# Kernel optimization log

Measured on AMD Instinct MI355X. Metric: run time of the kernel, lower is better.

## Reference

```python
import jax, jax.numpy as jnp
import numpy as np

NEG_SLOPE = 0.2
LN_EPS = 1e-5


def setup_inputs() -> dict:
    key = jax.random.key(0)
    k1, k2, k3, k4 = jax.random.split(key, 4)
    N, E, Din, Dout = 50000, 1000000, 64, 64
    h = jax.random.normal(k1, (N, Din), dtype=jnp.float32)
    edge_index = jax.random.randint(k2, (2, E), 0, N, dtype=jnp.int32)
    # Linear(in_dim, out_dim, bias=False): weight [Dout, Din]
    W = jax.random.normal(k3, (Dout, Din), dtype=jnp.float32) / np.sqrt(Din)
    # attention vector a: [1, 2*Dout] (xavier-normal-ish scale)
    a = jax.random.normal(k4, (1, 2 * Dout), dtype=jnp.float32) * 0.1
    ln_gamma = jnp.ones((Dout,), dtype=jnp.float32)
    ln_beta = jnp.zeros((Dout,), dtype=jnp.float32)
    return {"h": h, "edge_index": edge_index, "W": W, "a": a,
            "ln_gamma": ln_gamma, "ln_beta": ln_beta}


def reference(h, edge_index, W, a, ln_gamma, ln_beta):
    N, Dout = h.shape[0], W.shape[0]
    src, dst = edge_index[0], edge_index[1]
    hW = h @ W.T  # [N, Dout]
    # score_e = leakyrelu([h_src || h_dst] . a) = leakyrelu(s1[src] + s2[dst])
    a1, a2 = a[0, :Dout], a[0, Dout:]
    s1 = hW @ a1  # [N]
    s2 = hW @ a2  # [N]
    e = jax.nn.leaky_relu(s1[src] + s2[dst], NEG_SLOPE)  # [E]
    # softmax grouped by source node (segment softmax), numerically stable
    m = jax.ops.segment_max(e, src, num_segments=N)  # [N]
    ex = jnp.exp(e - m[src])
    denom = jax.ops.segment_sum(ex, src, num_segments=N)  # [N]
    att = ex / denom[src]  # [E]  (dropout: eval mode, identity)
    # scatter-add weighted source features into destination nodes
    msg = att[:, None] * hW[src]  # [E, Dout]
    h_prime = jnp.zeros_like(hW).at[dst].add(msg)
    # residual + LayerNorm
    x = hW + h_prime
    mu = jnp.mean(x, axis=-1, keepdims=True)
    var = jnp.var(x, axis=-1, keepdims=True)
    return (x - mu) * jax.lax.rsqrt(var + LN_EPS) * ln_gamma + ln_beta
```

## Files before the change

### kernel.cpp

```cpp
#include <hip/hip_runtime.h>
#include <hip/hip_bf16.h>

#define NEG_SLOPE 0.2f
#define LN_EPS 1e-5f
#define D 64
#define BSH 6
#define BNODES 64
#define NBMAX 1024
#define BCAP 1792
#define SSH 8
#define NSBMAX 256
#define SCAP 6144
#define OVFCAP 65536

typedef unsigned long long u64;
typedef unsigned int u32;
typedef unsigned short u16;

__device__ __forceinline__ u16 f2bf(float f) {
    u32 u = __float_as_uint(f);
    return (u16)((u + 0x7FFFu + ((u >> 16) & 1u)) >> 16);
}
__device__ __forceinline__ float bf_lo(u32 p) { return __uint_as_float(p << 16); }
__device__ __forceinline__ float bf_hi(u32 p) { return __uint_as_float(p & 0xFFFF0000u); }

__global__ void __launch_bounds__(256, 4)
k_hw_scores(const float* __restrict__ h,
            const float* __restrict__ W,
            const float* __restrict__ a,
            float* __restrict__ hW,
            u16* __restrict__ hWb,
            float* __restrict__ s1,
            float* __restrict__ s2,
            int N) {
    const int lane = threadIdx.x & 63;
    const int wid  = threadIdx.x >> 6;
    const int wavesPerBlock = blockDim.x >> 6;
    const int nWaves = gridDim.x * wavesPerBlock;

    float wcol[D];
    {
        const float4* wr = (const float4*)(W + (size_t)lane * D);
        #pragma unroll
        for (int q = 0; q < D / 4; ++q) {
            float4 w4 = wr[q];
            wcol[q * 4 + 0] = w4.x; wcol[q * 4 + 1] = w4.y;
            wcol[q * 4 + 2] = w4.z; wcol[q * 4 + 3] = w4.w;
        }
    }
    const float a1l = a[lane];
    const float a2l = a[D + lane];

    for (int i = blockIdx.x * wavesPerBlock + wid; i < N; i += nWaves) {
        const int iu = __builtin_amdgcn_readfirstlane(i);
        const float* hr = h + (size_t)iu * D;

        float acc0 = 0.f, acc1 = 0.f, acc2 = 0.f, acc3 = 0.f;
        #pragma unroll
        for (int k = 0; k < D; k += 4) {
            acc0 = fmaf(hr[k + 0], wcol[k + 0], acc0);
            acc1 = fmaf(hr[k + 1], wcol[k + 1], acc1);
            acc2 = fmaf(hr[k + 2], wcol[k + 2], acc2);
            acc3 = fmaf(hr[k + 3], wcol[k + 3], acc3);
        }
        float c = (acc0 + acc1) + (acc2 + acc3);
        hW[(size_t)iu * D + lane] = c;
        hWb[(size_t)iu * D + lane] = f2bf(c);

        float p1 = c * a1l;
        float p2 = c * a2l;
        #pragma unroll
        for (int off = 32; off > 0; off >>= 1) {
            p1 += __shfl_xor(p1, off, 64);
            p2 += __shfl_xor(p2, off, 64);
        }
        if (lane == 0) { s1[iu] = p1; s2[iu] = p2; }
    }
}

__device__ __forceinline__ float edge_ex(float v1, float v2) {
    float x = v1 + v2;
    float e = x > 0.f ? x : NEG_SLOPE * x;
    return expf(fminf(e, 60.f));
}

__global__ void __launch_bounds__(1024)
k_bin(const int* __restrict__ src,
      const int* __restrict__ dst,
      const float* __restrict__ s1,
      const float* __restrict__ s2,
      float* __restrict__ denom,
      int* __restrict__ dcnt_g,
      u32* __restrict__ drecs,
      int* __restrict__ scnt_g,
      u32* __restrict__ srecs,
      u32* __restrict__ ovf_rec,
      int* __restrict__ ovf_dst,
      int* __restrict__ ovf_n,
      int E, int nb, int nsb) {
    const int TPB = 1024, EPT = 4;
    __shared__ int lcnt[NBMAX], lbase[NBMAX], lfill[NBMAX];
    __shared__ int scnt[NSBMAX], sbase[NSBMAX], sfill[NSBMAX];

    const int chunk = blockIdx.x * (TPB * EPT);
    for (int i = threadIdx.x; i < nb; i += TPB)  { lcnt[i] = 0; lfill[i] = 0; }
    for (int i = threadIdx.x; i < nsb; i += TPB) { scnt[i] = 0; sfill[i] = 0; }
    __syncthreads();

    int sv[EPT], dv[EPT];
    const int e0 = chunk + threadIdx.x * EPT;
    if (e0 + EPT <= E) {
        int4 s4 = *(const int4*)(src + e0);
        int4 d4 = *(const int4*)(dst + e0);
        sv[0] = s4.x; sv[1] = s4.y; sv[2] = s4.z; sv[3] = s4.w;
        dv[0] = d4.x; dv[1] = d4.y; dv[2] = d4.z; dv[3] = d4.w;
    } else {
        #pragma unroll
        for (int j = 0; j < EPT; ++j) {
            int i = e0 + j;
            sv[j] = (i < E) ? src[i] : 0;
            dv[j] = (i < E) ? dst[i] : -1;
        }
    }

    #pragma unroll
    for (int j = 0; j < EPT; ++j) {
        if (dv[j] >= 0) {
            atomicAdd(&lcnt[dv[j] >> BSH], 1);
            atomicAdd(&scnt[sv[j] >> SSH], 1);
        }
    }
    __syncthreads();

    for (int b = threadIdx.x; b < nb; b += TPB) {
        int l = lcnt[b];
        if (l) lbase[b] = atomicAdd(&dcnt_g[b], l);
    }
    for (int b = threadIdx.x; b < nsb; b += TPB) {
        int l = scnt[b];
        if (l) sbase[b] = atomicAdd(&scnt_g[b], l);
    }
    __syncthreads();

    #pragma unroll
    for (int j = 0; j < EPT; ++j) {
        int d_ = dv[j];
        if (d_ < 0) continue;
        int s = sv[j];

        int b = d_ >> BSH;
        u32 drec = (u32)s | ((u32)(d_ & (BNODES - 1)) << 16);
        int r = lbase[b] + atomicAdd(&lfill[b], 1);
        if (r < BCAP) {
            drecs[(size_t)b * BCAP + r] = drec;
        } else {
            int o = atomicAdd(ovf_n, 1);
            if (o < OVFCAP) { ovf_rec[o] = drec; ovf_dst[o] = d_; }
        }

        int sb = s >> SSH;
        u32 srec = (u32)s | ((u32)d_ << 16);
        int rs = sbase[sb] + atomicAdd(&sfill[sb], 1);
        if (rs < SCAP) {
            srecs[(size_t)sb * SCAP + rs] = srec;
        } else {
            atomicAdd(&denom[s], edge_ex(s1[s], s2[d_]));
        }
    }
}

__global__ void __launch_bounds__(512)
k_denom(const u32* __restrict__ srecs,
        const int* __restrict__ scnt_g,
        const float* __restrict__ s1,
        const float* __restrict__ s2,
        float* __restrict__ denom,
        int N) {
    __shared__ float acc[256];
    const int b = blockIdx.x;
    const int tid = threadIdx.x;
    if (tid < 256) acc[tid] = 0.f;
    __syncthreads();

    const int total = min(scnt_g[b], SCAP);
    const u32* base = srecs + (size_t)b * SCAP;
    for (int i = tid; i < total; i += 512) {
        u32 r = base[i];
        int s = r & 0xFFFF;
        int d = r >> 16;
        atomicAdd(&acc[s & 255], edge_ex(s1[s], s2[d]));
    }
    __syncthreads();

    if (tid < 256) {
        int g = (b << SSH) + tid;
        if (g < N) denom[g] += acc[tid];
    }
}

__global__ void __launch_bounds__(512)
k_bucket_agg(const u32* __restrict__ drecs,
             const int* __restrict__ dcnt_g,
             const float* __restrict__ s1,
             const float* __restrict__ s2,
             const float* __restrict__ denom,
             const float* __restrict__ hW,
             const u16* __restrict__ hWb,
             const float* __restrict__ gamma,
             const float* __restrict__ beta,
             const u32* __restrict__ ovf_rec,
             const int* __restrict__ ovf_dst,
             const int* __restrict__ ovf_n_p,
             float* __restrict__ out,
             int N) {
    __shared__ u64 ro[BCAP];
    __shared__ float s2l[BNODES];
    __shared__ int hh[BNODES], oo[BNODES], cc[BNODES];

    const int b    = blockIdx.x;
    const int tid  = threadIdx.x;
    const int lane = tid & 63;
    const int wid  = tid >> 6;
    const int g    = lane >> 4;
    const int li   = lane & 15;
    const int node0 = b << BSH;
    const int nn    = min(BNODES, N - node0);
    const int total = min(dcnt_g[b], BCAP);

    if (tid < nn) s2l[tid] = s2[node0 + tid];
    if (tid < BNODES) hh[tid] = 0;
    __syncthreads();

    u64 rr[4]; bool valid[4];
    const u32* base = drecs + (size_t)b * BCAP;
    #pragma unroll
    for (int q = 0; q < 4; ++q) {
        int idx = tid + q * 512;
        valid[q] = idx < total;
        u32 r = valid[q] ? base[idx] : 0u;
        if (valid[q]) {
            int s  = r & 0xFFFF;
            int dl = (r >> 16) & (BNODES - 1);
            float att = edge_ex(s1[s], s2l[dl]) / denom[s];
            rr[q] = ((u64)__float_as_uint(att) << 32) | (u64)r;
            atomicAdd(&hh[dl], 1);
        } else rr[q] = 0;
    }
    __syncthreads();

    if (tid < BNODES) oo[tid] = hh[tid];
    __syncthreads();
    for (int off = 1; off < BNODES; off <<= 1) {
        int t = 0;
        if (tid < BNODES && tid >= off) t = oo[tid - off];
        __syncthreads();
        if (tid < BNODES) oo[tid] += t;
        __syncthreads();
    }
    if (tid < BNODES) { int e_ = oo[tid] - hh[tid]; oo[tid] = e_; cc[tid] = e_; }
    __syncthreads();

    #pragma unroll
    for (int q = 0; q < 4; ++q) if (valid[q])
        ro[atomicAdd(&cc[((u32)rr[q] >> 16) & (BNODES - 1)], 1)] = rr[q];
    __syncthreads();

    int ovn = *ovf_n_p;
    if (ovn > OVFCAP) ovn = OVFCAP;

    #pragma unroll
    for (int k = 0; k < 8; ++k) {
        int nl = (wid << 3) + k;
        if (nl >= nn) break;
        int beg = oo[nl], end = cc[nl];

        float ax = 0.f, ay = 0.f, az = 0.f, aw = 0.f;
        for (int p = beg; p < end; p += 16) {
            float at0 = 0.f, at1 = 0.f, at2 = 0.f, at3 = 0.f;
            int s0 = 0, s1i = 0, s2i = 0, s3 = 0;
            int i0 = p + g, i1 = p + 4 + g, i2 = p + 8 + g, i3 = p + 12 + g;
            if (i0 < end) { u64 r2 = ro[i0]; s0  = (u32)r2 & 0xFFFF; at0 = __uint_as_float((u32)(r2 >> 32)); }
            if (i1 < end) { u64 r2 = ro[i1]; s1i = (u32)r2 & 0xFFFF; at1 = __uint_as_float((u32)(r2 >> 32)); }
            if (i2 < end) { u64 r2 = ro[i2]; s2i = (u32)r2 & 0xFFFF; at2 = __uint_as_float((u32)(r2 >> 32)); }
            if (i3 < end) { u64 r2 = ro[i3]; s3  = (u32)r2 & 0xFFFF; at3 = __uint_as_float((u32)(r2 >> 32)); }
            const uint2 v0 = *(const uint2*)(hWb + (size_t)s0  * D + li * 4);
            const uint2 v1 = *(const uint2*)(hWb + (size_t)s1i * D + li * 4);
            const uint2 v2 = *(const uint2*)(hWb + (size_t)s2i * D + li * 4);
            const uint2 v3 = *(const uint2*)(hWb + (size_t)s3  * D + li * 4);
            ax = fmaf(at0, bf_lo(v0.x), ax); ay = fmaf(at0, bf_hi(v0.x), ay);
            az = fmaf(at0, bf_lo(v0.y), az); aw = fmaf(at0, bf_hi(v0.y), aw);
            ax = fmaf(at1, bf_lo(v1.x), ax); ay = fmaf(at1, bf_hi(v1.x), ay);
            az = fmaf(at1, bf_lo(v1.y), az); aw = fmaf(at1, bf_hi(v1.y), aw);
            ax = fmaf(at2, bf_lo(v2.x), ax); ay = fmaf(at2, bf_hi(v2.x), ay);
            az = fmaf(at2, bf_lo(v2.y), az); aw = fmaf(at2, bf_hi(v2.y), aw);
            ax = fmaf(at3, bf_lo(v3.x), ax); ay = fmaf(at3, bf_hi(v3.x), ay);
            az = fmaf(at3, bf_lo(v3.y), az); aw = fmaf(at3, bf_hi(v3.y), aw);
        }

        for (int r = 0; r < ovn; ++r) {
            if (ovf_dst[r] != node0 + nl) continue;
            if (g == 0) {
                u32 r2 = ovf_rec[r];
                int s = r2 & 0xFFFF;
                float att = edge_ex(s1[s], s2l[nl]) / denom[s];
                const uint2 v = *(const uint2*)(hWb + (size_t)s * D + li * 4);
                ax = fmaf(att, bf_lo(v.x), ax); ay = fmaf(att, bf_hi(v.x), ay);
                az = fmaf(att, bf_lo(v.y), az); aw = fmaf(att, bf_hi(v.y), aw);
            }
        }

        ax += __shfl_xor(ax, 16, 64); ax += __shfl_xor(ax, 32, 64);
        ay += __shfl_xor(ay, 16, 64); ay += __shfl_xor(ay, 32, 64);
        az += __shfl_xor(az, 16, 64); az += __shfl_xor(az, 32, 64);
        aw += __shfl_xor(aw, 16, 64); aw += __shfl_xor(aw, 32, 64);

        const float4 hv = *(const float4*)(hW + (size_t)(node0 + nl) * D + li * 4);
        float x0 = hv.x + ax, x1 = hv.y + ay, x2 = hv.z + az, x3 = hv.w + aw;

        float sm = x0 + x1 + x2 + x3;
        sm += __shfl_xor(sm, 1, 64); sm += __shfl_xor(sm, 2, 64);
        sm += __shfl_xor(sm, 4, 64); sm += __shfl_xor(sm, 8, 64);
        float mu = sm * (1.f / D);
        float d0 = x0 - mu, d1 = x1 - mu, d2 = x2 - mu, d3 = x3 - mu;
        float vv = d0 * d0 + d1 * d1 + d2 * d2 + d3 * d3;
        vv += __shfl_xor(vv, 1, 64); vv += __shfl_xor(vv, 2, 64);
        vv += __shfl_xor(vv, 4, 64); vv += __shfl_xor(vv, 8, 64);
        float inv = rsqrtf(vv * (1.f / D) + LN_EPS);

        if (g == 0) {
            const float4 gm = *(const float4*)(gamma + li * 4);
            const float4 bt = *(const float4*)(beta + li * 4);
            float4 o;
            o.x = d0 * inv * gm.x + bt.x;
            o.y = d1 * inv * gm.y + bt.y;
            o.z = d2 * inv * gm.z + bt.z;
            o.w = d3 * inv * gm.w + bt.w;
            *(float4*)(out + (size_t)(node0 + nl) * D + li * 4) = o;
        }
    }
}

static inline size_t align256(size_t x) { return (x + 255) & ~size_t(255); }

extern "C" void kernel_launch(void* const* d_in, const int* in_sizes, int n_in,
                              void* d_out, int out_size, void* d_ws, size_t ws_size,
                              hipStream_t stream) {
    const float* h    = (const float*)d_in[0];
    const int*   ei   = (const int*)d_in[1];
    const float* W    = (const float*)d_in[2];
    const float* a    = (const float*)d_in[3];
    const float* lng  = (const float*)d_in[4];
    const float* lnb  = (const float*)d_in[5];
    float* out = (float*)d_out;

    const int N = in_sizes[0] / D;
    const int E = in_sizes[1] / 2;
    const int* src = ei;
    const int* dst = ei + E;
    const int nb  = (N + BNODES - 1) >> BSH;
    const int nsb = (N + 255) >> SSH;

    char* ws = (char*)d_ws;
    size_t off = 0;
    float* hW      = (float*)(ws + off); off += align256(sizeof(float) * (size_t)N * D);
    u16*   hWb     = (u16*)  (ws + off); off += align256(sizeof(u16) * (size_t)N * D);
    float* s1      = (float*)(ws + off); off += align256(sizeof(float) * (size_t)N);
    float* s2      = (float*)(ws + off); off += align256(sizeof(float) * (size_t)N);
    u32*   drecs   = (u32*)  (ws + off); off += align256(sizeof(u32) * (size_t)nb * BCAP);
    u32*   srecs   = (u32*)  (ws + off); off += align256(sizeof(u32) * (size_t)nsb * SCAP);
    u32*   ovf_rec = (u32*)  (ws + off); off += align256(sizeof(u32) * (size_t)OVFCAP);
    int*   ovf_dst = (int*)  (ws + off); off += align256(sizeof(int) * (size_t)OVFCAP);
    size_t zero_off = off;
    float* denom   = (float*)(ws + off); off += align256(sizeof(float) * (size_t)N);
    int*   dcnt_g  = (int*)  (ws + off); off += align256(sizeof(int) * (size_t)NBMAX);
    int*   scnt_g  = (int*)  (ws + off); off += align256(sizeof(int) * (size_t)NSBMAX);
    int*   ovf_n   = (int*)  (ws + off); off += align256(sizeof(int));
    size_t zero_bytes = off - zero_off;

    hipMemsetAsync(ws + zero_off, 0, zero_bytes, stream);

    k_hw_scores<<<dim3(1024), dim3(256), 0, stream>>>(h, W, a, hW, hWb, s1, s2, N);

    k_bin<<<dim3((E + 4095) / 4096), dim3(1024), 0, stream>>>(
        src, dst, s1, s2, denom, dcnt_g, drecs, scnt_g, srecs,
        ovf_rec, ovf_dst, ovf_n, E, nb, nsb);

    k_denom<<<dim3(nsb), dim3(512), 0, stream>>>(srecs, scnt_g, s1, s2, denom, N);

    k_bucket_agg<<<dim3(nb), dim3(512), 0, stream>>>(
        drecs, dcnt_g, s1, s2, denom, hW, hWb, lng, lnb,
        ovf_rec, ovf_dst, ovf_n, out, N);
}
```

Measured before the change: 164.3 us.

## Stage edge records through a shared-memory counting sort before writing global bins

The binning kernel first counting-sorts its chunk of edges by bucket in shared memory, using a block-wide prefix scan. It then writes each bucket's records to global memory as contiguous runs. This replaces scattered per-edge stores that each needed their own shared-memory atomic slot. The destination and source binning passes now run one after the other and share the same shared buffers, which adds more barriers and two log-step scans. Destination records also carry the bucket index in their top bits, so downstream readers must mask those bits.

```diff
diff --git a/kernel.cpp b/kernel.cpp
--- a/kernel.cpp
+++ b/kernel.cpp
@@ -99,16 +99,15 @@
       int* __restrict__ ovf_n,
       int E, int nb, int nsb) {
     const int TPB = 1024, EPT = 4;
-    __shared__ int lcnt[NBMAX], lbase[NBMAX], lfill[NBMAX];
-    __shared__ int scnt[NSBMAX], sbase[NSBMAX], sfill[NSBMAX];
-
+    __shared__ u32 recbuf[TPB * EPT];
+    __shared__ int lcnt[NBMAX], lo[NBMAX], cc[NBMAX], lbase[NBMAX];
+
+    const int tid = threadIdx.x;
     const int chunk = blockIdx.x * (TPB * EPT);
-    for (int i = threadIdx.x; i < nb; i += TPB)  { lcnt[i] = 0; lfill[i] = 0; }
-    for (int i = threadIdx.x; i < nsb; i += TPB) { scnt[i] = 0; sfill[i] = 0; }
-    __syncthreads();
+    const int total = min(E - chunk, TPB * EPT);
 
     int sv[EPT], dv[EPT];
-    const int e0 = chunk + threadIdx.x * EPT;
+    const int e0 = chunk + tid * EPT;
     if (e0 + EPT <= E) {
         int4 s4 = *(const int4*)(src + e0);
         int4 d4 = *(const int4*)(dst + e0);
@@ -123,48 +122,95 @@
         }
     }
 
+    for (int i = tid; i < nb; i += TPB) lcnt[i] = 0;
+    __syncthreads();
+    #pragma unroll
+    for (int j = 0; j < EPT; ++j)
+        if (dv[j] >= 0) atomicAdd(&lcnt[dv[j] >> BSH], 1);
+    __syncthreads();
+
+    if (tid < nb) lo[tid] = lcnt[tid];
+    __syncthreads();
+    for (int off = 1; off < nb; off <<= 1) {
+        int t = 0;
+        if (tid < nb && tid >= off) t = lo[tid - off];
+        __syncthreads();
+        if (tid < nb) lo[tid] += t;
+        __syncthreads();
+    }
+    if (tid < nb) {
+        int e_ = lo[tid] - lcnt[tid];
+        lo[tid] = e_; cc[tid] = e_;
+        if (lcnt[tid]) lbase[tid] = atomicAdd(&dcnt_g[tid], lcnt[tid]);
+    }
+    __syncthreads();
+
     #pragma unroll
     for (int j = 0; j < EPT; ++j) {
-        if (dv[j] >= 0) {
-            atomicAdd(&lcnt[dv[j] >> BSH], 1);
-            atomicAdd(&scnt[sv[j] >> SSH], 1);
-        }
-    }
-    __syncthreads();
-
-    for (int b = threadIdx.x; b < nb; b += TPB) {
-        int l = lcnt[b];
-        if (l) lbase[b] = atomicAdd(&dcnt_g[b], l);
-    }
-    for (int b = threadIdx.x; b < nsb; b += TPB) {
-        int l = scnt[b];
-        if (l) sbase[b] = atomicAdd(&scnt_g[b], l);
-    }
-    __syncthreads();
-
-    #pragma unroll
-    for (int j = 0; j < EPT; ++j) {
-        int d_ = dv[j];
-        if (d_ < 0) continue;
-        int s = sv[j];
-
-        int b = d_ >> BSH;
-        u32 drec = (u32)s | ((u32)(d_ & (BNODES - 1)) << 16);
-        int r = lbase[b] + atomicAdd(&lfill[b], 1);
+        if (dv[j] < 0) continue;
+        int b = dv[j] >> BSH;
+        u32 rec = (u32)sv[j] | ((u32)(dv[j] & (BNODES - 1)) << 16) | ((u32)b << 22);
+        recbuf[atomicAdd(&cc[b], 1)] = rec;
+    }
+    __syncthreads();
+
+    for (int i = tid; i < total; i += TPB) {
+        u32 rec = recbuf[i];
+        int b = rec >> 22;
+        int r = lbase[b] + (i - lo[b]);
         if (r < BCAP) {
-            drecs[(size_t)b * BCAP + r] = drec;
+            drecs[(size_t)b * BCAP + r] = rec;
         } else {
             int o = atomicAdd(ovf_n, 1);
-            if (o < OVFCAP) { ovf_rec[o] = drec; ovf_dst[o] = d_; }
-        }
-
-        int sb = s >> SSH;
-        u32 srec = (u32)s | ((u32)d_ << 16);
-        int rs = sbase[sb] + atomicAdd(&sfill[sb], 1);
-        if (rs < SCAP) {
-            srecs[(size_t)sb * SCAP + rs] = srec;
+            if (o < OVFCAP) {
+                ovf_rec[o] = rec;
+                ovf_dst[o] = (b << BSH) | ((rec >> 16) & (BNODES - 1));
+            }
+        }
+    }
+    __syncthreads();
+
+    for (int i = tid; i < nsb; i += TPB) lcnt[i] = 0;
+    __syncthreads();
+    #pragma unroll
+    for (int j = 0; j < EPT; ++j)
+        if (dv[j] >= 0) atomicAdd(&lcnt[sv[j] >> SSH], 1);
+    __syncthreads();
+
+    if (tid < nsb) lo[tid] = lcnt[tid];
+    __syncthreads();
+    for (int off = 1; off < nsb; off <<= 1) {
+        int t = 0;
+        if (tid < nsb && tid >= off) t = lo[tid - off];
+        __syncthreads();
+        if (tid < nsb) lo[tid] += t;
+        __syncthreads();
+    }
+    if (tid < nsb) {
+        int e_ = lo[tid] - lcnt[tid];
+        lo[tid] = e_; cc[tid] = e_;
+        if (lcnt[tid]) lbase[tid] = atomicAdd(&scnt_g[tid], lcnt[tid]);
+    }
+    __syncthreads();
+
+    #pragma unroll
+    for (int j = 0; j < EPT; ++j) {
+        if (dv[j] < 0) continue;
+        int b = sv[j] >> SSH;
+        u32 rec = (u32)sv[j] | ((u32)dv[j] << 16);
+        recbuf[atomicAdd(&cc[b], 1)] = rec;
+    }
+    __syncthreads();
+
+    for (int i = tid; i < total; i += TPB) {
+        u32 rec = recbuf[i];
+        int s = rec & 0xFFFF;
+        int b = s >> SSH;
+        int r = lbase[b] + (i - lo[b]);
+        if (r < SCAP) {
+            srecs[(size_t)b * SCAP + r] = rec;
         } else {
-            atomicAdd(&denom[s], edge_ex(s1[s], s2[d_]));
+            atomicAdd(&denom[s], edge_ex(s1[s], s2[rec >> 16]));
         }
     }
 }
```

Result: no change. 163.8 us (-0.3%).
